# Optimization experiments

Measured on AMD Instinct MI355X. Metric: run time of the kernel, lower is better.

Reference implementation:

```python
import jax, jax.numpy as jnp
import numpy as np

EPS = 1e-12
N_HEADS = 16


def _ln(x, g, b, eps=EPS):
    m = jnp.mean(x, axis=-1, keepdims=True)
    v = jnp.var(x, axis=-1, keepdims=True)
    return (x - m) * jax.lax.rsqrt(v + eps) * g + b


def setup_inputs() -> dict:
    key = jax.random.key(0)
    ks = jax.random.split(key, 8)
    B, S, D, I = 2, 2048, 1024, 4096
    s = 0.02
    f32 = jnp.float32
    return {
        "x": jax.random.normal(ks[0], (B, S, D), f32),
        "input_mask": jnp.zeros((B, 1, 1, S), f32),  # additive mask, 0 = no masking
        "norm_w": jnp.ones((D,), f32),
        "norm_b": jnp.zeros((D,), f32),
        "attn_qkvw": jax.random.normal(ks[1], (D, 3 * D), f32) * s,
        "attn_qkvb": jnp.zeros((3 * D,), f32),
        "attn_ow": jax.random.normal(ks[2], (D, D), f32) * s,
        "attn_ob": jnp.zeros((D,), f32),
        "attn_nw": jnp.ones((D,), f32),
        "attn_nb": jnp.zeros((D,), f32),
        "inter_w": jax.random.normal(ks[3], (D, I), f32) * s,
        "inter_b": jnp.zeros((I,), f32),
        "inter_w1": jax.random.normal(ks[4], (D, I), f32) * s,
        "output_w": jax.random.normal(ks[5], (I, D), f32) * s,
        "output_b": jnp.zeros((D,), f32),
    }


def reference(x, input_mask, norm_w, norm_b, attn_qkvw, attn_qkvb, attn_ow,
              attn_ob, attn_nw, attn_nb, inter_w, inter_b, inter_w1,
              output_w, output_b):
    B, S, D = x.shape
    hd = D // N_HEADS

    # --- fused qkv_gemm: pre-layernorm + QKV GEMM + bias ---
    ln1 = _ln(x, norm_w, norm_b)
    qkv = ln1 @ attn_qkvw + attn_qkvb            # [B,S,3D]
    q, k, v = jnp.split(qkv, 3, axis=-1)

    def to_heads(t):  # [B,S,D] -> [B,H,S,hd]
        return t.reshape(B, S, N_HEADS, hd).transpose(0, 2, 1, 3)

    q, k, v = to_heads(q), to_heads(k), to_heads(v)

    # --- softmax-context attention (scale_attention=True -> 1/sqrt(head_dim)) ---
    scores = jnp.einsum('bhqd,bhkd->bhqk', q, k) / jnp.sqrt(jnp.float32(hd))
    scores = scores + input_mask                 # additive mask [B,1,1,S]
    probs = jax.nn.softmax(scores, axis=-1)
    ctx = jnp.einsum('bhqk,bhkd->bhqd', probs, v)
    ctx = ctx.transpose(0, 2, 1, 3).reshape(B, S, D)

    attn_out = ctx @ attn_ow                     # vector_matmul (no bias)

    # --- fused mlp_gemm: bias+residual add, layernorm, GEMM+bias+gelu ---
    residual_add = attn_out + attn_ob + x
    ln2 = _ln(residual_add, attn_nw, attn_nb)
    intermediate = jax.nn.gelu(ln2 @ inter_w + inter_b, approximate=False)
    # gated path: vector_matmul(mlp input, inter_w1) * intermediate (per source)
    intermediate = (attn_out @ inter_w1) * intermediate

    # --- output projection + bias_residual ---
    out = intermediate @ output_w + output_b + residual_add
    return out
```

## Files before the change

kernel.cpp:

```cpp
#include <hip/hip_runtime.h>
#include <hip/hip_bf16.h>

#define BATCH 2
#define SEQ   2048
#define DIM   1024
#define IDIM  4096
#define NH    16
#define HD    64
#define TOK   (BATCH * SEQ)

typedef __hip_bfloat16 bf16;

typedef short bf16x8_t __attribute__((ext_vector_type(8)));
typedef float f32x4_t  __attribute__((ext_vector_type(4)));

__device__ __forceinline__ float ldv(const float* p, size_t i) { return p[i]; }
__device__ __forceinline__ float ldv(const bf16*  p, size_t i) { return __bfloat162float(p[i]); }
__device__ __forceinline__ void  stv(float* p, size_t i, float v) { p[i] = v; }
__device__ __forceinline__ void  stv(bf16*  p, size_t i, float v) { p[i] = __float2bfloat16(v); }

__device__ __forceinline__ f32x4_t mfma16(bf16x8_t a, bf16x8_t b, f32x4_t c) {
    return __builtin_amdgcn_mfma_f32_16x16x32_bf16(a, b, c, 0, 0, 0);
}

__device__ __forceinline__ void gload16(const bf16* g, bf16* l) {
    __builtin_amdgcn_global_load_lds(
        (const __attribute__((address_space(1))) void*)g,
        (__attribute__((address_space(3))) void*)l, 16, 0, 0);
}

__device__ __forceinline__ void xcd_map(int &bx, int &by) {
    const int gn  = gridDim.x;
    const int lin = blockIdx.y * gn + blockIdx.x;
    const int cx  = gn >> 3;
    const int xcd = lin & 7;
    const int slot = lin >> 3;
    bx = xcd * cx + slot % cx;
    by = slot / cx;
}

__global__ __launch_bounds__(256) void ln_kernel(const float* __restrict__ in,
                                                 const float* __restrict__ w,
                                                 const float* __restrict__ b,
                                                 bf16* __restrict__ out) {
    const int wid  = threadIdx.x >> 6;
    const int lane = threadIdx.x & 63;
    const int row  = blockIdx.x * 4 + wid;
    const float4* xr = (const float4*)(in + (size_t)row * DIM);

    float4 v[4];
    float sum = 0.f, sq = 0.f;
#pragma unroll
    for (int i = 0; i < 4; i++) {
        v[i] = xr[lane + i * 64];
        sum += v[i].x + v[i].y + v[i].z + v[i].w;
        sq  += v[i].x * v[i].x + v[i].y * v[i].y + v[i].z * v[i].z + v[i].w * v[i].w;
    }
#pragma unroll
    for (int off = 32; off >= 1; off >>= 1) {
        sum += __shfl_xor(sum, off);
        sq  += __shfl_xor(sq,  off);
    }

    const float mean = sum * (1.f / DIM);
    const float var  = fmaxf(sq * (1.f / DIM) - mean * mean, 0.f);
    const float rstd = rsqrtf(var + 1e-12f);

    const float4* wv = (const float4*)w;
    const float4* bv = (const float4*)b;
    ushort4* orow = (ushort4*)(out + (size_t)row * DIM);
#pragma unroll
    for (int i = 0; i < 4; i++) {
        const int c = lane + i * 64;
        const float4 wc = wv[c];
        const float4 bc = bv[c];
        ushort4 o;
        o.x = __bfloat16_as_ushort(__float2bfloat16((v[i].x - mean) * rstd * wc.x + bc.x));
        o.y = __bfloat16_as_ushort(__float2bfloat16((v[i].y - mean) * rstd * wc.y + bc.y));
        o.z = __bfloat16_as_ushort(__float2bfloat16((v[i].z - mean) * rstd * wc.z + bc.z));
        o.w = __bfloat16_as_ushort(__float2bfloat16((v[i].w - mean) * rstd * wc.w + bc.w));
        orow[c] = o;
    }
}

__global__ __launch_bounds__(256) void wconv5_kernel(const float* __restrict__ W0, bf16* __restrict__ T0,
                                                     const float* __restrict__ W1, bf16* __restrict__ T1,
                                                     const float* __restrict__ W2, bf16* __restrict__ T2,
                                                     const float* __restrict__ W3, bf16* __restrict__ T3,
                                                     const float* __restrict__ W4, bf16* __restrict__ T4) {
    __shared__ float tile[32][33];
    int bid = blockIdx.x;
    const float* W; bf16* T; int K, N;
    if (bid < 3072)       { W = W0; T = T0; K = 1024; N = 3072; }
    else if (bid < 4096)  { W = W1; T = T1; K = 1024; N = 1024; bid -= 3072; }
    else if (bid < 8192)  { W = W2; T = T2; K = 1024; N = 4096; bid -= 4096; }
    else if (bid < 12288) { W = W3; T = T3; K = 1024; N = 4096; bid -= 8192; }
    else                  { W = W4; T = T4; K = 4096; N = 1024; bid -= 12288; }
    const int ntx = N >> 5;
    const int n0 = (bid % ntx) * 32;
    const int k0 = (bid / ntx) * 32;

    const int tid = threadIdx.x;
    const int c = tid & 31;
    const int r = tid >> 5;
#pragma unroll
    for (int i = 0; i < 4; i++)
        tile[r + i * 8][c] = W[(size_t)(k0 + r + i * 8) * N + n0 + c];
    __syncthreads();
#pragma unroll
    for (int i = 0; i < 4; i++)
        T[(size_t)(n0 + r + i * 8) * K + k0 + c] = __float2bfloat16(tile[c][r + i * 8]);
}

#define GBK 32

template<typename TX, int MODE, int TM, int TN>
__global__ __launch_bounds__(256) void mgemm_kernel(const bf16* __restrict__ A,
                                                    const bf16* __restrict__ Bt,
                                                    const float* __restrict__ bias,
                                                    const TX* __restrict__ aux,
                                                    TX* __restrict__ C,
                                                    const float* __restrict__ bias2,
                                                    const float* __restrict__ xin,
                                                    float* __restrict__ C2,
                                                    int M, int N, int K) {
    constexpr int TILE_M = TM * 32;
    constexpr int TILE_N = TN * 32;
    constexpr int LOADS  = TM / 2 + TN / 2;
    __shared__ alignas(16) bf16 As[2][TILE_M][GBK];
    __shared__ alignas(16) bf16 Bs[2][TILE_N][GBK];

    const int tid  = threadIdx.x;
    const int w    = tid >> 6;
    const int lane = tid & 63;
    const int cl   = lane & 15;
    const int qd   = lane >> 4;
    const int wm   = w >> 1;
    const int wn   = w & 1;

    int bx, by;
    xcd_map(bx, by);

    const int row0 = by * TILE_M;
    const int col0 = bx * TILE_N;

    const int lrow = lane >> 2;
    const int lkg  = lane & 3;
    const int sslot = lkg ^ ((lrow >> 1) & 3);
    const int rds   = (cl >> 1) & 3;

    const bf16* gA = A  + (size_t)(row0 + lrow) * K + sslot * 8;
    const bf16* gB = Bt + (size_t)(col0 + lrow) * K + sslot * 8;

    f32x4_t acc[TM][TN];
#pragma unroll
    for (int m = 0; m < TM; m++)
#pragma unroll
        for (int n = 0; n < TN; n++) acc[m][n] = {0.f, 0.f, 0.f, 0.f};

    auto stage = [&](int b, int k0) {
#pragma unroll
        for (int i = 0; i < TM / 2; i++) {
            const int r16 = (w * (TM / 2) + i) * 16;
            gload16(gA + (size_t)r16 * K + k0, &As[b][r16][0]);
        }
#pragma unroll
        for (int j = 0; j < TN / 2; j++) {
            const int r16 = (w * (TN / 2) + j) * 16;
            gload16(gB + (size_t)r16 * K + k0, &Bs[b][r16][0]);
        }
    };

    stage(0, 0);
    stage(1, GBK);
    asm volatile("s_waitcnt vmcnt(%0)" :: "i"(LOADS) : "memory");
    __builtin_amdgcn_s_barrier();

    const int NT = K / GBK;
    for (int t = 0; t < NT; t++) {
        const int cur = t & 1;

        bf16x8_t af[TM], bfr[TN];
#pragma unroll
        for (int m = 0; m < TM; m++)
            af[m] = *(const bf16x8_t*)&As[cur][wm * (TM * 16) + m * 16 + cl][(qd ^ rds) * 8];
#pragma unroll
        for (int n = 0; n < TN; n++)
            bfr[n] = *(const bf16x8_t*)&Bs[cur][wn * (TN * 16) + n * 16 + cl][(qd ^ rds) * 8];
        asm volatile("s_waitcnt lgkmcnt(0)" ::: "memory");
        __builtin_amdgcn_sched_barrier(0);
        __builtin_amdgcn_s_barrier();

        if (t + 2 < NT) stage(cur, (t + 2) * GBK);

        __builtin_amdgcn_s_setprio(1);
#pragma unroll
        for (int m = 0; m < TM; m++)
#pragma unroll
            for (int n = 0; n < TN; n++)
                acc[m][n] = mfma16(af[m], bfr[n], acc[m][n]);
        __builtin_amdgcn_s_setprio(0);

        if (t + 1 < NT) {
            if (t + 2 < NT)
                asm volatile("s_waitcnt vmcnt(%0)" :: "i"(LOADS) : "memory");
            else
                asm volatile("s_waitcnt vmcnt(0)" ::: "memory");
            __builtin_amdgcn_s_barrier();
        }
    }

#pragma unroll
    for (int m = 0; m < TM; m++) {
#pragma unroll
        for (int n = 0; n < TN; n++) {
            const int gc = col0 + wn * (TN * 16) + n * 16 + cl;
            const float bv = (MODE != 4 && bias) ? bias[gc] : 0.f;
#pragma unroll
            for (int r = 0; r < 4; r++) {
                const int gr = row0 + wm * (TM * 16) + m * 16 + qd * 4 + r;
                float c = acc[m][n][r] + bv;
                if (MODE == 3) {
                    c += ldv(aux, (size_t)gr * N + gc);
                }
                stv(C, (size_t)gr * N + gc, c);
                if (MODE == 4) {
                    C2[(size_t)gr * N + gc] = c + bias2[gc] + xin[(size_t)gr * N + gc];
                }
            }
        }
    }
}

__global__ __launch_bounds__(512, 4) void dualgemm_kernel(const bf16* __restrict__ A0,
                                                          const bf16* __restrict__ B0t,
                                                          const bf16* __restrict__ A1,
                                                          const bf16* __restrict__ B1t,
                                                          const float* __restrict__ bias,
                                                          bf16* __restrict__ C,
                                                          int M, int N, int K) {
    __shared__ alignas(16) char pool[66560];

    const int tid  = threadIdx.x;
    const int w    = tid >> 6;
    const int lane = tid & 63;
    const int cl   = lane & 15;
    const int qd   = lane >> 4;
    const int gsel = w >> 2;
    const int g2   = w & 3;
    const int wm   = g2 >> 1;
    const int wn   = g2 & 1;

    int bx, by;
    xcd_map(bx, by);
    const int row0 = by * 128;
    const int col0 = bx * 128;

    const int lrow = lane >> 2;
    const int lkg  = lane & 3;
    const int sslot = lkg ^ ((lrow >> 1) & 3);
    const int rds   = (cl >> 1) & 3;

    const int sarr = w >> 1;
    const bf16* gsrc;
    {
        const bf16* bases[4] = {A0, B0t, A1, B1t};
        const int   r0s[4]   = {row0, col0, row0, col0};
        gsrc = bases[sarr] + (size_t)(r0s[sarr] + lrow) * K + sslot * 8;
    }

    auto sptr = [&](int b, int a) -> bf16* {
        return (bf16*)(pool + b * 32768 + a * 8192);
    };

    f32x4_t acc[4][4];
#pragma unroll
    for (int m = 0; m < 4; m++)
#pragma unroll
        for (int n = 0; n < 4; n++) acc[m][n] = {0.f, 0.f, 0.f, 0.f};

    auto stage = [&](int b, int k0) {
        bf16* dst = sptr(b, sarr);
#pragma unroll
        for (int j = 0; j < 4; j++) {
            const int rg = (w & 1) * 4 + j;
            gload16(gsrc + (size_t)(rg * 16) * K + k0, dst + rg * 16 * GBK);
        }
    };

    stage(0, 0);
    stage(1, GBK);
    asm volatile("s_waitcnt vmcnt(4)" ::: "memory");
    __builtin_amdgcn_s_barrier();

    const int NT = K / GBK;
    for (int t = 0; t < NT; t++) {
        const int cur = t & 1;
        const bf16* Sa = sptr(cur, gsel * 2);
        const bf16* Sb = sptr(cur, gsel * 2 + 1);

        bf16x8_t af[4], bfr[4];
#pragma unroll
        for (int m = 0; m < 4; m++)
            af[m] = *(const bf16x8_t*)&Sa[(wm * 64 + m * 16 + cl) * GBK + (qd ^ rds) * 8];
#pragma unroll
        for (int n = 0; n < 4; n++)
            bfr[n] = *(const bf16x8_t*)&Sb[(wn * 64 + n * 16 + cl) * GBK + (qd ^ rds) * 8];
        asm volatile("s_waitcnt lgkmcnt(0)" ::: "memory");
        __builtin_amdgcn_sched_barrier(0);
        __builtin_amdgcn_s_barrier();

        if (t + 2 < NT) stage(cur, (t + 2) * GBK);

        __builtin_amdgcn_s_setprio(1);
#pragma unroll
        for (int m = 0; m < 4; m++)
#pragma unroll
            for (int n = 0; n < 4; n++)
                acc[m][n] = mfma16(af[m], bfr[n], acc[m][n]);
        __builtin_amdgcn_s_setprio(0);

        if (t + 1 < NT) {
            if (t + 2 < NT)
                asm volatile("s_waitcnt vmcnt(4)" ::: "memory");
            else
                asm volatile("s_waitcnt vmcnt(0)" ::: "memory");
            __builtin_amdgcn_s_barrier();
        }
    }

    float* X = (float*)pool;
    __syncthreads();
    if (gsel == 1) {
#pragma unroll
        for (int m = 0; m < 4; m++)
#pragma unroll
            for (int n = 0; n < 4; n++)
#pragma unroll
                for (int r = 0; r < 4; r++)
                    X[(wm * 64 + m * 16 + qd * 4 + r) * 130 + wn * 64 + n * 16 + cl] =
                        acc[m][n][r];
    }
    __syncthreads();
    if (gsel == 0) {
#pragma unroll
        for (int m = 0; m < 4; m++) {
#pragma unroll
            for (int n = 0; n < 4; n++) {
                const int lc = wn * 64 + n * 16 + cl;
                const int gc = col0 + lc;
                const float bv = bias[gc];
#pragma unroll
                for (int r = 0; r < 4; r++) {
                    const int lr = wm * 64 + m * 16 + qd * 4 + r;
                    float g = acc[m][n][r] + bv;
                    g = 0.5f * g * (1.f + erff(g * 0.70710678118654752f));
                    C[(size_t)(row0 + lr) * N + gc] = __float2bfloat16(g * X[lr * 130 + lc]);
                }
            }
        }
    }
}

__global__ __launch_bounds__(256) void vtrans_kernel(const bf16* __restrict__ qkv,
                                                     bf16* __restrict__ vt) {
    __shared__ bf16 t[64][72];
    const int tid = threadIdx.x;
    const int s0  = blockIdx.x * 64;
    const int bh  = blockIdx.y;
    const int bb  = bh >> 4;
    const int h   = bh & 15;
    const bf16* src = qkv + (size_t)bb * SEQ * (3 * DIM) + 2 * DIM + h * HD;
    const int r  = tid >> 3;
    const int cc = tid & 7;
#pragma unroll
    for (int i = 0; i < 2; i++)
        *(bf16x8_t*)&t[r + i * 32][cc * 8] =
            *(const bf16x8_t*)(src + (size_t)(s0 + r + i * 32) * (3 * DIM) + cc * 8);
    __syncthreads();
    bf16* dst = vt + (size_t)bh * HD * SEQ + s0;
#pragma unroll
    for (int i = 0; i < 2; i++) {
        const int d = r + i * 32;
        bf16x8_t v;
#pragma unroll
        for (int j = 0; j < 8; j++)
            ((short*)&v)[j] = *(const short*)&t[cc * 8 + j][d];
        *(bf16x8_t*)(dst + (size_t)d * SEQ + cc * 8) = v;
    }
}

#define KCH 64
#define NCH (SEQ / KCH)

__device__ __forceinline__ unsigned pk2(float lo, float hi) {
    unsigned a = (unsigned)__bfloat16_as_ushort(__float2bfloat16(lo));
    unsigned b = (unsigned)__bfloat16_as_ushort(__float2bfloat16(hi));
    return a | (b << 16);
}

union PAU { bf16x8_t v; unsigned u[4]; };

__global__ __launch_bounds__(256, 2) void attn_mfma_kernel(const bf16* __restrict__ qkv,
                                                           const bf16* __restrict__ vt,
                                                           const float* __restrict__ mask,
                                                           bf16* __restrict__ ctx) {
    __shared__ alignas(16) bf16 Kl[2][KCH][64];
    __shared__ alignas(16) bf16 Vl[2][KCH][64];

    const int tid  = threadIdx.x;
    const int w    = tid >> 6;
    const int lane = tid & 63;
    const int cl   = lane & 15;
    const int qd   = lane >> 4;
    const int c7   = cl & 7;

    const int qtile = blockIdx.x;
    const int bh    = blockIdx.y;
    const int bb    = bh >> 4;
    const int h     = bh & 15;

    const bf16*  base = qkv + (size_t)bb * SEQ * (3 * DIM) + h * HD;
    const bf16*  gK   = base + DIM;
    const bf16*  gV   = vt + (size_t)bh * HD * SEQ;
    const float* mrow = mask + (size_t)bb * SEQ;

    bf16x8_t aq[2][2];
#pragma unroll
    for (int qt = 0; qt < 2; qt++) {
        const bf16* qrow = base + (size_t)(qtile * 128 + w * 32 + qt * 16 + cl) * (3 * DIM);
        aq[qt][0] = *(const bf16x8_t*)(qrow + qd * 8);
        aq[qt][1] = *(const bf16x8_t*)(qrow + 32 + qd * 8);
    }

    const bf16x8_t onesv = {0x3F80, 0x3F80, 0x3F80, 0x3F80,
                            0x3F80, 0x3F80, 0x3F80, 0x3F80};

    const int sr  = lane >> 3;
    const int scw = (lane & 7) ^ sr;

#pragma unroll
    for (int i = 0; i < 2; i++) {
        const int row = i * 32 + w * 8 + sr;
        gload16(gK + (size_t)row * (3 * DIM) + scw * 8, &Kl[0][i * 32 + w * 8][0]);
        gload16(gV + (size_t)row * SEQ + scw * 8, &Vl[0][i * 32 + w * 8][0]);
    }
    f32x4_t mkx[4];
#pragma unroll
    for (int ks = 0; ks < 4; ks++)
        mkx[ks] = *(const f32x4_t*)&mrow[ks * 16 + qd * 4];

    f32x4_t O[2][4];
#pragma unroll
    for (int qt = 0; qt < 2; qt++)
#pragma unroll
        for (int ns = 0; ns < 4; ns++) O[qt][ns] = {0.f, 0.f, 0.f, 0.f};
    f32x4_t li[2] = {{0.f,0.f,0.f,0.f},{0.f,0.f,0.f,0.f}};

    for (int c = 0; c < NCH; c++) {
        __syncthreads();
        const bf16 (*Kb)[64] = Kl[c & 1];
        const bf16 (*Vb)[64] = Vl[c & 1];

        f32x4_t mk[4];
#pragma unroll
        for (int ks = 0; ks < 4; ks++) mk[ks] = mkx[ks];

        if (c + 1 < NCH) {
            bf16 (*Kn)[64] = Kl[(c + 1) & 1];
            bf16 (*Vn)[64] = Vl[(c + 1) & 1];
            const int k0n = (c + 1) * KCH;
#pragma unroll
            for (int i = 0; i < 2; i++) {
                const int row = i * 32 + w * 8 + sr;
                gload16(gK + (size_t)(k0n + row) * (3 * DIM) + scw * 8, &Kn[i * 32 + w * 8][0]);
                gload16(gV + (size_t)row * SEQ + k0n + scw * 8, &Vn[i * 32 + w * 8][0]);
            }
#pragma unroll
            for (int ks = 0; ks < 4; ks++)
                mkx[ks] = *(const f32x4_t*)&mrow[k0n + ks * 16 + qd * 4];
        }

        bf16x8_t kf[4][2];
#pragma unroll
        for (int ks = 0; ks < 4; ks++) {
            kf[ks][0] = *(const bf16x8_t*)&Kb[ks * 16 + cl][(qd ^ c7) << 3];
            kf[ks][1] = *(const bf16x8_t*)&Kb[ks * 16 + cl][((4 + qd) ^ c7) << 3];
        }

        PAU pa[2][2];
#pragma unroll
        for (int qt = 0; qt < 2; qt++) {
            unsigned Dv[4][2];
#pragma unroll
            for (int ks = 0; ks < 4; ks++) {
                f32x4_t s = {0.f, 0.f, 0.f, 0.f};
                s = mfma16(kf[ks][0], aq[qt][0], s);
                s = mfma16(kf[ks][1], aq[qt][1], s);
                const float e0 = __expf(s[0] * 0.125f + mk[ks][0]);
                const float e1 = __expf(s[1] * 0.125f + mk[ks][1]);
                const float e2 = __expf(s[2] * 0.125f + mk[ks][2]);
                const float e3 = __expf(s[3] * 0.125f + mk[ks][3]);
                Dv[ks][0] = pk2(e0, e1);
                Dv[ks][1] = pk2(e2, e3);
            }
#pragma unroll
            for (int rp = 0; rp < 2; rp++) {
                auto z0 = __builtin_amdgcn_permlane32_swap(Dv[0][rp], Dv[1][rp], false, false);
                auto w0 = __builtin_amdgcn_permlane16_swap(z0[0], z0[1], false, false);
                pa[qt][0].u[rp]     = w0[0];
                pa[qt][0].u[rp + 2] = w0[1];
                auto z1 = __builtin_amdgcn_permlane32_swap(Dv[2][rp], Dv[3][rp], false, false);
                auto w1 = __builtin_amdgcn_permlane16_swap(z1[0], z1[1], false, false);
                pa[qt][1].u[rp]     = w1[0];
                pa[qt][1].u[rp + 2] = w1[1];
            }
            f32x4_t ls = {0.f, 0.f, 0.f, 0.f};
            ls = mfma16(pa[qt][0].v, onesv, ls);
            ls = mfma16(pa[qt][1].v, onesv, ls);
            li[qt] += ls;
        }

#pragma unroll
        for (int ns = 0; ns < 4; ns++) {
            bf16x8_t v0 = *(const bf16x8_t*)&Vb[ns * 16 + cl][(qd ^ c7) << 3];
            bf16x8_t v1 = *(const bf16x8_t*)&Vb[ns * 16 + cl][((4 + qd) ^ c7) << 3];
#pragma unroll
            for (int qt = 0; qt < 2; qt++) {
                O[qt][ns] = mfma16(pa[qt][0].v, v0, O[qt][ns]);
                O[qt][ns] = mfma16(pa[qt][1].v, v1, O[qt][ns]);
            }
        }
    }

#pragma unroll
    for (int qt = 0; qt < 2; qt++) {
#pragma unroll
        for (int r = 0; r < 4; r++) {
            const int row = qtile * 128 + w * 32 + qt * 16 + qd * 4 + r;
            bf16* orow = ctx + (size_t)(bb * SEQ + row) * DIM + h * HD;
            const float inv = 1.f / li[qt][r];
#pragma unroll
            for (int ns = 0; ns < 4; ns++)
                orow[ns * 16 + cl] = __float2bfloat16(O[qt][ns][r] * inv);
        }
    }
}

extern "C" void kernel_launch(void* const* d_in, const int* in_sizes, int n_in,
                              void* d_out, int out_size, void* d_ws, size_t ws_size,
                              hipStream_t stream) {
    const float* x        = (const float*)d_in[0];
    const float* mask     = (const float*)d_in[1];
    const float* norm_w   = (const float*)d_in[2];
    const float* norm_b   = (const float*)d_in[3];
    const float* qkvw     = (const float*)d_in[4];
    const float* qkvb     = (const float*)d_in[5];
    const float* attn_ow  = (const float*)d_in[6];
    const float* attn_ob  = (const float*)d_in[7];
    const float* attn_nw  = (const float*)d_in[8];
    const float* attn_nb  = (const float*)d_in[9];
    const float* inter_w  = (const float*)d_in[10];
    const float* inter_b  = (const float*)d_in[11];
    const float* inter_w1 = (const float*)d_in[12];
    const float* output_w = (const float*)d_in[13];
    const float* output_b = (const float*)d_in[14];

    float* out = (float*)d_out;
    bf16*  ws  = (bf16*)d_ws;

    const size_t M1 = 1024 * 1024;
    bf16* ln_s      = ws;
    bf16* qkv       = ws + 4 * M1;
    bf16* inter     = ws + 4 * M1;
    bf16* qkvw_t    = ws + 16 * M1;
    bf16* attn_owt  = ws + 19 * M1;
    bf16* vt        = ws + 20 * M1;
    bf16* attn_out  = ws + 20 * M1;
    bf16* inter_wt  = ws + 24 * M1;
    bf16* inter_w1t = ws + 28 * M1;
    bf16* output_wt = ws + 32 * M1;
    float* resid    = out;

    dim3 blk(256);
    dim3 blk512(512);

    wconv5_kernel<<<dim3(16384), blk, 0, stream>>>(
        qkvw, qkvw_t, attn_ow, attn_owt, inter_w, inter_wt,
        inter_w1, inter_w1t, output_w, output_wt);

    ln_kernel<<<TOK / 4, blk, 0, stream>>>(x, norm_w, norm_b, ln_s);

    mgemm_kernel<bf16, 0, 4, 4><<<dim3(3072 / 128, TOK / 128), blk, 0, stream>>>(
        ln_s, qkvw_t, qkvb, (const bf16*)nullptr, qkv,
        nullptr, nullptr, nullptr, TOK, 3 * DIM, DIM);

    vtrans_kernel<<<dim3(SEQ / 64, BATCH * NH), blk, 0, stream>>>(qkv, vt);

    attn_mfma_kernel<<<dim3(SEQ / 128, BATCH * NH), blk, 0, stream>>>(qkv, vt, mask, ln_s);

    mgemm_kernel<bf16, 4, 4, 2><<<dim3(DIM / 64, TOK / 128), blk, 0, stream>>>(
        ln_s, attn_owt, (const float*)nullptr, (const bf16*)nullptr, attn_out,
        attn_ob, x, resid, TOK, DIM, DIM);

    ln_kernel<<<TOK / 4, blk, 0, stream>>>(resid, attn_nw, attn_nb, ln_s);

    dualgemm_kernel<<<dim3(IDIM / 128, TOK / 128), blk512, 0, stream>>>(
        ln_s, inter_wt, attn_out, inter_w1t, inter_b, inter, TOK, IDIM, DIM);

    mgemm_kernel<float, 3, 4, 2><<<dim3(DIM / 64, TOK / 128), blk, 0, stream>>>(
        inter, output_wt, output_b, resid, out,
        nullptr, nullptr, nullptr, TOK, DIM, IDIM);
}
```

Before: 431.4 us.

## Fuse V-transpose into QKV GEMM epilogue, merge LN into weight conversion, reorder barriers

Removes the separate V-transpose kernel: the QKV GEMM epilogue now writes V columns directly in transposed [B,H,D,S] layout as packed 4-element stores. The first layernorm is folded into the weight-conversion launch as extra blocks, saving one launch. The GEMM main loops drop the lgkmcnt wait plus barrier placed before the MFMAs and instead barrier after the MFMAs before staging the next tile, which shortens the time between LDS reads and compute. The remaining risk is the LDS ordering in the new schedule: the stage write into the buffer just read relies on the post-MFMA barrier.

Result: slower. 451.8 us (+4.7%).

```diff
diff --git a/kernel.cpp b/kernel.cpp
--- a/kernel.cpp
+++ b/kernel.cpp
@@ -39,15 +39,12 @@
     by = slot / cx;
 }
 
-__global__ __launch_bounds__(256) void ln_kernel(const float* __restrict__ in,
-                                                 const float* __restrict__ w,
-                                                 const float* __restrict__ b,
-                                                 bf16* __restrict__ out) {
-    const int wid  = threadIdx.x >> 6;
-    const int lane = threadIdx.x & 63;
-    const int row  = blockIdx.x * 4 + wid;
+__device__ __forceinline__ void ln_one_row(const float* __restrict__ in,
+                                           const float* __restrict__ w,
+                                           const float* __restrict__ b,
+                                           bf16* __restrict__ out,
+                                           int row, int lane) {
     const float4* xr = (const float4*)(in + (size_t)row * DIM);
-
     float4 v[4];
     float sum = 0.f, sq = 0.f;
 #pragma unroll
@@ -61,7 +58,6 @@
         sum += __shfl_xor(sum, off);
         sq  += __shfl_xor(sq,  off);
     }
-
     const float mean = sum * (1.f / DIM);
     const float var  = fmaxf(sq * (1.f / DIM) - mean * mean, 0.f);
     const float rstd = rsqrtf(var + 1e-12f);
@@ -83,13 +79,28 @@
     }
 }
 
-__global__ __launch_bounds__(256) void wconv5_kernel(const float* __restrict__ W0, bf16* __restrict__ T0,
-                                                     const float* __restrict__ W1, bf16* __restrict__ T1,
-                                                     const float* __restrict__ W2, bf16* __restrict__ T2,
-                                                     const float* __restrict__ W3, bf16* __restrict__ T3,
-                                                     const float* __restrict__ W4, bf16* __restrict__ T4) {
+__global__ __launch_bounds__(256) void ln_kernel(const float* __restrict__ in,
+                                                 const float* __restrict__ w,
+                                                 const float* __restrict__ b,
+                                                 bf16* __restrict__ out) {
+    ln_one_row(in, w, b, out, blockIdx.x * 4 + (threadIdx.x >> 6), threadIdx.x & 63);
+}
+
+__global__ __launch_bounds__(256) void wconv5ln_kernel(
+        const float* __restrict__ W0, bf16* __restrict__ T0,
+        const float* __restrict__ W1, bf16* __restrict__ T1,
+        const float* __restrict__ W2, bf16* __restrict__ T2,
+        const float* __restrict__ W3, bf16* __restrict__ T3,
+        const float* __restrict__ W4, bf16* __restrict__ T4,
+        const float* __restrict__ x, const float* __restrict__ nw,
+        const float* __restrict__ nb, bf16* __restrict__ lnout) {
     __shared__ float tile[32][33];
     int bid = blockIdx.x;
+    if (bid >= 16384) {
+        ln_one_row(x, nw, nb, lnout,
+                   (bid - 16384) * 4 + (threadIdx.x >> 6), threadIdx.x & 63);
+        return;
+    }
     const float* W; bf16* T; int K, N;
     if (bid < 3072)       { W = W0; T = T0; K = 1024; N = 3072; }
     else if (bid < 4096)  { W = W1; T = T1; K = 1024; N = 1024; bid -= 3072; }
@@ -123,6 +134,7 @@
                                                     const float* __restrict__ bias2,
                                                     const float* __restrict__ xin,
                                                     float* __restrict__ C2,
+                                                    bf16* __restrict__ vtout,
                                                     int M, int N, int K) {
     constexpr int TILE_M = TM * 32;
     constexpr int TILE_N = TN * 32;
@@ -187,11 +199,6 @@
 #pragma unroll
         for (int n = 0; n < TN; n++)
             bfr[n] = *(const bf16x8_t*)&Bs[cur][wn * (TN * 16) + n * 16 + cl][(qd ^ rds) * 8];
-        asm volatile("s_waitcnt lgkmcnt(0)" ::: "memory");
-        __builtin_amdgcn_sched_barrier(0);
-        __builtin_amdgcn_s_barrier();
-
-        if (t + 2 < NT) stage(cur, (t + 2) * GBK);
 
         __builtin_amdgcn_s_setprio(1);
 #pragma unroll
@@ -201,6 +208,10 @@
                 acc[m][n] = mfma16(af[m], bfr[n], acc[m][n]);
         __builtin_amdgcn_s_setprio(0);
 
+        if (t + 2 < NT) {
+            __builtin_amdgcn_s_barrier();
+            stage(cur, (t + 2) * GBK);
+        }
         if (t + 1 < NT) {
             if (t + 2 < NT)
                 asm volatile("s_waitcnt vmcnt(%0)" :: "i"(LOADS) : "memory");
@@ -216,16 +227,33 @@
         for (int n = 0; n < TN; n++) {
             const int gc = col0 + wn * (TN * 16) + n * 16 + cl;
             const float bv = (MODE != 4 && bias) ? bias[gc] : 0.f;
+            const int grb = row0 + wm * (TM * 16) + m * 16 + qd * 4;
+            float cv[4];
 #pragma unroll
             for (int r = 0; r < 4; r++) {
-                const int gr = row0 + wm * (TM * 16) + m * 16 + qd * 4 + r;
                 float c = acc[m][n][r] + bv;
-                if (MODE == 3) {
-                    c += ldv(aux, (size_t)gr * N + gc);
-                }
-                stv(C, (size_t)gr * N + gc, c);
-                if (MODE == 4) {
-                    C2[(size_t)gr * N + gc] = c + bias2[gc] + xin[(size_t)gr * N + gc];
+                if (MODE == 3) c += ldv(aux, (size_t)(grb + r) * N + gc);
+                cv[r] = c;
+            }
+            if (MODE == 0 && vtout != nullptr && gc >= 2 * DIM) {
+                const int hv = (gc - 2 * DIM) >> 6;
+                const int dv = (gc - 2 * DIM) & 63;
+                const int bb = grb >> 11;
+                const int sb = grb & 2047;
+                ushort4 o;
+                o.x = __bfloat16_as_ushort(__float2bfloat16(cv[0]));
+                o.y = __bfloat16_as_ushort(__float2bfloat16(cv[1]));
+                o.z = __bfloat16_as_ushort(__float2bfloat16(cv[2]));
+                o.w = __bfloat16_as_ushort(__float2bfloat16(cv[3]));
+                *(ushort4*)(vtout + (((size_t)(bb * NH + hv)) << 17) +
+                            ((size_t)dv << 11) + sb) = o;
+            } else {
+#pragma unroll
+                for (int r = 0; r < 4; r++) {
+                    stv(C, (size_t)(grb + r) * N + gc, cv[r]);
+                    if (MODE == 4)
+                        C2[(size_t)(grb + r) * N + gc] =
+                            cv[r] + bias2[gc] + xin[(size_t)(grb + r) * N + gc];
                 }
             }
         }
@@ -306,11 +334,6 @@
 #pragma unroll
         for (int n = 0; n < 4; n++)
             bfr[n] = *(const bf16x8_t*)&Sb[(wn * 64 + n * 16 + cl) * GBK + (qd ^ rds) * 8];
-        asm volatile("s_waitcnt lgkmcnt(0)" ::: "memory");
-        __builtin_amdgcn_sched_barrier(0);
-        __builtin_amdgcn_s_barrier();
-
-        if (t + 2 < NT) stage(cur, (t + 2) * GBK);
 
         __builtin_amdgcn_s_setprio(1);
 #pragma unroll
@@ -320,6 +343,10 @@
                 acc[m][n] = mfma16(af[m], bfr[n], acc[m][n]);
         __builtin_amdgcn_s_setprio(0);
 
+        if (t + 2 < NT) {
+            __builtin_amdgcn_s_barrier();
+            stage(cur, (t + 2) * GBK);
+        }
         if (t + 1 < NT) {
             if (t + 2 < NT)
                 asm volatile("s_waitcnt vmcnt(4)" ::: "memory");
@@ -359,34 +386,6 @@
                 }
             }
         }
-    }
-}
-
-__global__ __launch_bounds__(256) void vtrans_kernel(const bf16* __restrict__ qkv,
-                                                     bf16* __restrict__ vt) {
-    __shared__ bf16 t[64][72];
-    const int tid = threadIdx.x;
-    const int s0  = blockIdx.x * 64;
-    const int bh  = blockIdx.y;
-    const int bb  = bh >> 4;
-    const int h   = bh & 15;
-    const bf16* src = qkv + (size_t)bb * SEQ * (3 * DIM) + 2 * DIM + h * HD;
-    const int r  = tid >> 3;
-    const int cc = tid & 7;
-#pragma unroll
-    for (int i = 0; i < 2; i++)
-        *(bf16x8_t*)&t[r + i * 32][cc * 8] =
-            *(const bf16x8_t*)(src + (size_t)(s0 + r + i * 32) * (3 * DIM) + cc * 8);
-    __syncthreads();
-    bf16* dst = vt + (size_t)bh * HD * SEQ + s0;
-#pragma unroll
-    for (int i = 0; i < 2; i++) {
-        const int d = r + i * 32;
-        bf16x8_t v;
-#pragma unroll
-        for (int j = 0; j < 8; j++)
-            ((short*)&v)[j] = *(const short*)&t[cc * 8 + j][d];
-        *(bf16x8_t*)(dst + (size_t)d * SEQ + cc * 8) = v;
     }
 }
 
@@ -585,23 +584,20 @@
     dim3 blk(256);
     dim3 blk512(512);
 
-    wconv5_kernel<<<dim3(16384), blk, 0, stream>>>(
+    wconv5ln_kernel<<<dim3(16384 + TOK / 4), blk, 0, stream>>>(
         qkvw, qkvw_t, attn_ow, attn_owt, inter_w, inter_wt,
-        inter_w1, inter_w1t, output_w, output_wt);
-
-    ln_kernel<<<TOK / 4, blk, 0, stream>>>(x, norm_w, norm_b, ln_s);
+        inter_w1, inter_w1t, output_w, output_wt,
+        x, norm_w, norm_b, ln_s);
 
     mgemm_kernel<bf16, 0, 4, 4><<<dim3(3072 / 128, TOK / 128), blk, 0, stream>>>(
         ln_s, qkvw_t, qkvb, (const bf16*)nullptr, qkv,
-        nullptr, nullptr, nullptr, TOK, 3 * DIM, DIM);
-
-    vtrans_kernel<<<dim3(SEQ / 64, BATCH * NH), blk, 0, stream>>>(qkv, vt);
+        nullptr, nullptr, nullptr, vt, TOK, 3 * DIM, DIM);
 
     attn_mfma_kernel<<<dim3(SEQ / 128, BATCH * NH), blk, 0, stream>>>(qkv, vt, mask, ln_s);
 
     mgemm_kernel<bf16, 4, 4, 2><<<dim3(DIM / 64, TOK / 128), blk, 0, stream>>>(
         ln_s, attn_owt, (const float*)nullptr, (const bf16*)nullptr, attn_out,
-        attn_ob, x, resid, TOK, DIM, DIM);
+        attn_ob, x, resid, nullptr, TOK, DIM, DIM);
 
     ln_kernel<<<TOK / 4, blk, 0, stream>>>(resid, attn_nw, attn_nb, ln_s);
 
@@ -610,5 +606,5 @@
 
     mgemm_kernel<float, 3, 4, 2><<<dim3(DIM / 64, TOK / 128), blk, 0, stream>>>(
         inter, output_wt, output_b, resid, out,
-        nullptr, nullptr, nullptr, TOK, DIM, IDIM);
-}
+        nullptr, nullptr, nullptr, nullptr, TOK, DIM, IDIM);
+}
```
